# Kernel optimization log

Measured on AMD Instinct MI355X. Metric: run time of the kernel, lower is better.

Reference implementation:

```python
import jax, jax.numpy as jnp
from jax import lax
import numpy as np

NUM_CLASSES = 80
STRIDES = (8, 16, 32)
CONF_THRE = 0.01
NMS_THRE = 0.65
TOPK = 500  # fixed pre-NMS candidate cap (jit-compatible stand-in for dynamic conf filter)


def setup_inputs() -> dict:
    key = jax.random.key(0)
    k8, k16, k32 = jax.random.split(key, 3)
    B, C = 8, 5 + NUM_CLASSES
    return {
        "out8": jax.random.normal(k8, (B, C, 160, 160), dtype=jnp.float32),
        "out16": jax.random.normal(k16, (B, C, 80, 80), dtype=jnp.float32),
        "out32": jax.random.normal(k32, (B, C, 40, 40), dtype=jnp.float32),
    }


def _decode_level(x, stride):
    # x: [B, C, H, W] -> decoded [B, H*W, C]
    B, C, H, W = x.shape
    x = x.reshape(B, C, H * W).transpose(0, 2, 1)  # [B, HW, C]
    yv, xv = jnp.meshgrid(jnp.arange(H), jnp.arange(W), indexing="ij")
    grid = jnp.stack([xv, yv], axis=-1).reshape(1, H * W, 2).astype(x.dtype)
    s = jnp.asarray(stride, x.dtype)
    xy = (x[..., 0:2] + grid) * s
    wh = jnp.exp(x[..., 2:4]) * s
    obj = jax.nn.sigmoid(x[..., 4:5])
    cls = jax.nn.sigmoid(x[..., 5:])
    return jnp.concatenate([xy, wh, obj, cls], axis=-1)


def _iou_one_vs_all(box, boxes):
    # box: [4] xyxy, boxes: [K,4] xyxy
    x1 = jnp.maximum(box[0], boxes[:, 0])
    y1 = jnp.maximum(box[1], boxes[:, 1])
    x2 = jnp.minimum(box[2], boxes[:, 2])
    y2 = jnp.minimum(box[3], boxes[:, 3])
    inter = jnp.maximum(x2 - x1, 0.0) * jnp.maximum(y2 - y1, 0.0)
    a1 = jnp.maximum(box[2] - box[0], 0.0) * jnp.maximum(box[3] - box[1], 0.0)
    a2 = jnp.maximum(boxes[:, 2] - boxes[:, 0], 0.0) * jnp.maximum(boxes[:, 3] - boxes[:, 1], 0.0)
    return inter / (a1 + a2 - inter + 1e-9)


def _nms_keep(boxes, valid, iou_thr):
    # boxes are pre-sorted by descending score; returns bool keep mask [K]
    K = boxes.shape[0]
    idx = jnp.arange(K)

    def body(i, state):
        keep, suppressed = state
        cur_ok = jnp.logical_not(suppressed[i])
        keep = keep.at[i].set(cur_ok)
        iou = _iou_one_vs_all(boxes[i], boxes)
        suppressed = suppressed | ((iou > iou_thr) & cur_ok & (idx > i))
        return keep, suppressed

    keep, _ = lax.fori_loop(0, K, body, (jnp.zeros(K, bool), jnp.logical_not(valid)))
    return keep


def _post_process_image(pred):
    # pred: [N, 5+num_classes] decoded, boxes already xyxy
    cls_scores = pred[:, 5:5 + NUM_CLASSES]
    class_conf = jnp.max(cls_scores, axis=1)
    class_pred = jnp.argmax(cls_scores, axis=1)
    obj = pred[:, 4]
    total = obj * class_conf  # NMS score, same as torchvision call
    masked = jnp.where(total >= CONF_THRE, total, -1.0)
    top_sc, top_i = lax.top_k(masked, TOPK)  # sorted descending
    boxes = pred[top_i, :4]
    obj_k = obj[top_i]
    cc_k = class_conf[top_i]
    lab_k = class_pred[top_i]
    valid = top_sc >= CONF_THRE
    # class-aware (batched) NMS via per-class coordinate offset, as torchvision does
    max_c = jnp.max(jnp.where(valid[:, None], boxes, 0.0)) + 1.0
    boxes_off = boxes + (lab_k.astype(boxes.dtype) * max_c)[:, None]
    keep = _nms_keep(boxes_off, valid, NMS_THRE)
    det = jnp.concatenate(
        [boxes, obj_k[:, None], cc_k[:, None], lab_k.astype(boxes.dtype)[:, None]], axis=1
    )  # [K, 7] = (x1,y1,x2,y2,obj,class_conf,class_id)
    return det * keep[:, None].astype(det.dtype)


def reference(out8, out16, out32):
    levels = [(out8, 8), (out16, 16), (out32, 32)]
    pred = jnp.concatenate([_decode_level(x, s) for x, s in levels], axis=1)  # [B, N, C]
    # cxcywh -> xyxy corners
    cx, cy, w, h = pred[..., 0], pred[..., 1], pred[..., 2], pred[..., 3]
    corners = jnp.stack([cx - w / 2, cy - h / 2, cx + w / 2, cy + h / 2], axis=-1)
    pred = jnp.concatenate([corners, pred[..., 4:]], axis=-1)
    return jax.vmap(_post_process_image)(pred)  # [B, TOPK, 7], zero-padded
```

## Files before the change

### kernel.cpp

```cpp
#include <hip/hip_runtime.h>

#define NPI    33600
#define KTOP   500
#define CAP    1024
#define KEY001 0xBC23D70Au
#define NGRP   1024
#define NIMG   8
#define GPW    525

__device__ __forceinline__ float sigmoidf_(float x) {
  return 1.0f / (1.0f + expf(-x));
}
__device__ __forceinline__ unsigned fkey(float f) {
  unsigned u = __float_as_uint(f);
  return (u & 0x80000000u) ? ~u : (u | 0x80000000u);
}

__global__ __launch_bounds__(256) void k_score(
    const float* __restrict__ p8, const float* __restrict__ p16,
    const float* __restrict__ p32,
    unsigned* __restrict__ keys, unsigned* __restrict__ hist2)
{
  const int b  = blockIdx.y;
  const int tx = blockIdx.x;
  const float* lvl; int HW, j0, abase;
  if (tx < 50)      { lvl = p8;  HW = 25600; j0 = tx * 512;        abase = 0; }
  else if (tx < 63) { lvl = p16; HW = 6400;  j0 = (tx - 50) * 512; abase = 25600; }
  else              { lvl = p32; HW = 1600;  j0 = (tx - 63) * 512; abase = 32000; }
  __shared__ unsigned lh[NGRP];
  for (int i = threadIdx.x; i < NGRP; i += 256) lh[i] = 0;
  __syncthreads();

  const int e = j0 + 2 * threadIdx.x;
  if (e < HW) {
    const float* base = lvl + (size_t)b * 85 * HW + e;
    float2 o2 = *(const float2*)(base + (size_t)4 * HW);
    float m0 = -INFINITY, m1 = -INFINITY;
    for (int c0 = 5; c0 < 85; c0 += 16) {
      float2 r[16];
      #pragma unroll
      for (int u = 0; u < 16; ++u)
        r[u] = *(const float2*)(base + (size_t)(c0 + u) * HW);
      #pragma unroll
      for (int u = 0; u < 16; ++u) { m0 = fmaxf(m0, r[u].x); m1 = fmaxf(m1, r[u].y); }
    }
    float s0 = sigmoidf_(o2.x) * sigmoidf_(m0);
    float s1 = sigmoidf_(o2.y) * sigmoidf_(m1);
    unsigned k0 = fkey(s0 >= 0.01f ? s0 : -1.0f);
    unsigned k1 = fkey(s1 >= 0.01f ? s1 : -1.0f);
    *(uint2*)(keys + (size_t)b * NPI + abase + e) = make_uint2(k0, k1);
    atomicAdd(&lh[k0 >> 22], 1u);
    atomicAdd(&lh[k1 >> 22], 1u);
  }
  __syncthreads();
  unsigned* gb = hist2 + (size_t)b * NGRP;
  for (int i = threadIdx.x; i < NGRP; i += 256) {
    unsigned v = lh[i];
    if (v) atomicAdd(&gb[i], v);
  }
}

__global__ __launch_bounds__(1024) void k_select(
    const unsigned* __restrict__ hist2, const unsigned* __restrict__ keys,
    unsigned* __restrict__ selanch, unsigned* __restrict__ invalg)
{
  const int b    = blockIdx.x;
  const int tid  = threadIdx.x;
  const int lane = tid & 63;
  const int wave = tid >> 6;

  __shared__ unsigned lh[NGRP];
  __shared__ unsigned sh_sub[4096];
  __shared__ unsigned sh_c64[64];
  __shared__ unsigned sh_G, sh_T;
  __shared__ __align__(16) unsigned long long sh_cand[CAP];
  __shared__ unsigned sh_inval[16];
  __shared__ unsigned sh_wcA[16], sh_wcB[16];

  lh[tid] = hist2[(size_t)b * NGRP + tid];
  for (int i = tid; i < 4096; i += 1024) sh_sub[i] = 0;
  __syncthreads();
  if (tid < 64) {
    unsigned s = 0;
    #pragma unroll
    for (int k = 0; k < 16; ++k) s += lh[tid * 16 + k];
    sh_c64[tid] = s;
  }
  __syncthreads();
  if (tid == 0) {
    unsigned cum = 0; int C = 0;
    for (int g = 63; g >= 0; --g) {
      unsigned v = sh_c64[g];
      if (cum + v >= KTOP) { C = g; break; }
      cum += v;
    }
    int G = C * 16; unsigned chi = cum;
    for (int g = C * 16 + 15; g >= C * 16; --g) {
      unsigned v = lh[g];
      if (chi + v >= KTOP) { G = g; break; }
      chi += v;
    }
    sh_G = (unsigned)G;
    sh_c64[0] = chi;
  }
  __syncthreads();
  const unsigned G = sh_G;
  const unsigned* kb = keys + (size_t)b * NPI;

  for (int g = tid; g < NPI / 4; g += 1024) {
    uint4 kv = ((const uint4*)kb)[g];
    unsigned kk[4] = {kv.x, kv.y, kv.z, kv.w};
    #pragma unroll
    for (int q = 0; q < 4; ++q)
      if ((kk[q] >> 22) == G) atomicAdd(&sh_sub[(kk[q] >> 10) & 4095u], 1u);
  }
  __syncthreads();
  unsigned chi10 = sh_c64[0];
  __syncthreads();
  if (tid < 64) {
    unsigned s = 0;
    for (int k = 0; k < 64; ++k) s += sh_sub[tid * 64 + k];
    sh_c64[tid] = s;
  }
  __syncthreads();
  if (tid == 0) {
    unsigned c = chi10; int C2 = 0;
    for (int g = 63; g >= 0; --g) {
      unsigned v = sh_c64[g];
      if (c + v >= KTOP) { C2 = g; break; }
      c += v;
    }
    int T12 = C2 * 64;
    for (int t2 = C2 * 64 + 63; t2 >= C2 * 64; --t2) {
      unsigned v = sh_sub[t2];
      if (c + v >= KTOP) { T12 = t2; break; }
      c += v;
    }
    sh_T = (G << 12) | (unsigned)T12;
  }
  __syncthreads();
  const unsigned T = sh_T;

  unsigned runA = 0, runB = 0;
  for (int it = 0; it < 9; ++it) {
    int gl = it * 64 + lane;
    bool act = (gl < GPW);
    int g = wave * GPW + gl;
    uint4 kv = act ? ((const uint4*)kb)[g] : make_uint4(0, 0, 0, 0);
    unsigned kk[4] = {kv.x, kv.y, kv.z, kv.w};
    #pragma unroll
    for (int q = 0; q < 4; ++q) {
      unsigned bin = kk[q] >> 10;
      runA += (unsigned)__popcll(__ballot(act && (bin > T)));
      runB += (unsigned)__popcll(__ballot(act && (bin == T)));
    }
  }
  if (lane == 0) { sh_wcA[wave] = runA; sh_wcB[wave] = runB; }
  __syncthreads();
  unsigned pA = 0, pB = 0, nA = 0, nBtot = 0;
  #pragma unroll
  for (int w2 = 0; w2 < 16; ++w2) {
    unsigned va = sh_wcA[w2], vb = sh_wcB[w2];
    if (w2 < wave) { pA += va; pB += vb; }
    nA += va; nBtot += vb;
  }
  const unsigned Bcap = CAP - nA;
  const unsigned nBk  = (nBtot < Bcap) ? nBtot : Bcap;
  const int nTot = (int)(nA + nBk);

  for (int it = 0; it < 9; ++it) {
    int gl = it * 64 + lane;
    bool act = (gl < GPW);
    int g = wave * GPW + gl;
    uint4 kv = act ? ((const uint4*)kb)[g] : make_uint4(0, 0, 0, 0);
    unsigned kk[4] = {kv.x, kv.y, kv.z, kv.w};
    bool iA[4], iB[4];
    unsigned long long balA[4], balB[4];
    #pragma unroll
    for (int q = 0; q < 4; ++q) {
      unsigned bin = kk[q] >> 10;
      iA[q] = act && (bin > T);
      iB[q] = act && (bin == T);
      balA[q] = __ballot(iA[q]);
      balB[q] = __ballot(iB[q]);
    }
    unsigned long long lt = (1ULL << lane) - 1ULL;
    unsigned pAl = pA, pBl = pB;
    #pragma unroll
    for (int q = 0; q < 4; ++q) {
      pAl += (unsigned)__popcll(balA[q] & lt);
      pBl += (unsigned)__popcll(balB[q] & lt);
    }
    #pragma unroll
    for (int q = 0; q < 4; ++q) {
      int a0 = g * 4 + q;
      unsigned long long packed =
          ((unsigned long long)kk[q] << 32) |
          (unsigned long long)(0xFFFFFFFFu - (unsigned)a0);
      if (iA[q]) { sh_cand[pAl] = packed; ++pAl; }
      if (iB[q]) { if (pBl < Bcap) sh_cand[nA + pBl] = packed; ++pBl; }
      pA += (unsigned)__popcll(balA[q]);
      pB += (unsigned)__popcll(balB[q]);
    }
  }
  __syncthreads();
  for (int s = nTot + tid; s < CAP; s += 1024) sh_cand[s] = 0ULL;
  __syncthreads();

  for (unsigned kk2 = 2; kk2 <= CAP; kk2 <<= 1) {
    for (unsigned jj = kk2 >> 1; jj > 0; jj >>= 1) {
      unsigned i = (unsigned)tid, p = i ^ jj;
      if (p > i) {
        unsigned long long x = sh_cand[i], y = sh_cand[p];
        bool desc = ((i & kk2) == 0);
        if ((x < y) == desc) { sh_cand[i] = y; sh_cand[p] = x; }
      }
      __syncthreads();
    }
  }

  if (tid < KTOP) {
    unsigned long long v = sh_cand[tid];
    unsigned keyk = (unsigned)(v >> 32);
    int a = (int)(0xFFFFFFFFu - (unsigned)(v & 0xFFFFFFFFull));
    if (a < 0) a = 0;
    selanch[b * KTOP + tid] = (unsigned)a;
    bool validk = (keyk >= KEY001);
    unsigned long long bv = __ballot(!validk);
    if (lane == 0) {
      sh_inval[wave * 2]     = (unsigned)(bv & 0xFFFFFFFFull);
      sh_inval[wave * 2 + 1] = (unsigned)(bv >> 32);
    }
  } else {
    unsigned long long bv = __ballot(false);
    (void)bv;
  }
  __syncthreads();
  if (tid < 16) invalg[b * 16 + tid] = sh_inval[tid];
}

__global__ __launch_bounds__(256) void k_gather(
    const float* __restrict__ p8, const float* __restrict__ p16,
    const float* __restrict__ p32,
    const unsigned* __restrict__ selanch, float* __restrict__ seldet)
{
  const int b    = blockIdx.y;
  const int part = blockIdx.x;
  const int tid  = threadIdx.x;
  const int p    = tid & 15;
  const int grp  = tid >> 4;
  const int lane = tid & 63;
  const int g0   = lane & ~15;

  for (int iter = 0; iter < 4; ++iter) {
    int s = part * 64 + iter * 16 + grp;
    if (s >= KTOP) continue;
    int a = (int)selanch[b * KTOP + s];
    const float* lvl; int j, W, HW, S;
    if (a < 25600)      { lvl = p8;  j = a;         W = 160; HW = 25600; S = 8;  }
    else if (a < 32000) { lvl = p16; j = a - 25600; W = 80;  HW = 6400;  S = 16; }
    else                { lvl = p32; j = a - 32000; W = 40;  HW = 1600;  S = 32; }
    const float* base = lvl + (size_t)b * 85 * HW + j;
    float cc = -1.0f; int lab = 0;
    #pragma unroll
    for (int u = 0; u < 5; ++u) {
      int c = p + 16 * u;
      float sv = sigmoidf_(base[(size_t)(5 + c) * HW]);
      if (sv > cc) { cc = sv; lab = c; }
    }
    float tload = (p < 5) ? base[(size_t)p * HW] : 0.0f;
    #pragma unroll
    for (int off = 1; off < 16; off <<= 1) {
      float occ = __shfl_xor(cc, off);
      int  olb = __shfl_xor(lab, off);
      if (occ > cc || (occ == cc && olb < lab)) { cc = occ; lab = olb; }
    }
    float t0 = __shfl(tload, g0 + 0);
    float t1 = __shfl(tload, g0 + 1);
    float t2 = __shfl(tload, g0 + 2);
    float t3 = __shfl(tload, g0 + 3);
    float t4 = __shfl(tload, g0 + 4);
    if (p == 0) {
      int gy = j / W, gx = j - gy * W;
      float fs = (float)S;
      float cx = (t0 + (float)gx) * fs;
      float cy = (t1 + (float)gy) * fs;
      float w  = expf(t2) * fs;
      float h  = expf(t3) * fs;
      float obj = sigmoidf_(t4);
      float* d = seldet + ((size_t)b * KTOP + s) * 7;
      d[0] = cx - 0.5f * w; d[1] = cy - 0.5f * h;
      d[2] = cx + 0.5f * w; d[3] = cy + 0.5f * h;
      d[4] = obj; d[5] = cc; d[6] = (float)lab;
    }
  }
}

__global__ __launch_bounds__(256) void k_iou(
    const float* __restrict__ seldet, const unsigned* __restrict__ invalg,
    unsigned* __restrict__ gmask)
{
  const int w = blockIdx.x, b = blockIdx.y;
  const int tid = threadIdx.x;
  const int lane = tid & 63;
  const int wave = tid >> 6;
  __shared__ float sd[KTOP * 7];
  __shared__ float sx1[512], sy1[512], sx2[512], sy2[512], sa[512];
  __shared__ float sred[4];
  __shared__ float smaxc;
  for (int x = tid; x < KTOP * 7; x += 256)
    sd[x] = seldet[(size_t)b * (KTOP * 7) + x];
  __syncthreads();
  float contrib = 0.0f;
  for (int i = tid; i < KTOP; i += 256) {
    bool valid = ((invalg[b * 16 + (i >> 5)] >> (i & 31)) & 1u) == 0u;
    float m4 = fmaxf(fmaxf(sd[i * 7 + 0], sd[i * 7 + 1]),
                     fmaxf(sd[i * 7 + 2], sd[i * 7 + 3]));
    contrib = fmaxf(contrib, valid ? m4 : 0.0f);
  }
  #pragma unroll
  for (int off = 32; off > 0; off >>= 1) contrib = fmaxf(contrib, __shfl_xor(contrib, off));
  if (lane == 0) sred[wave] = contrib;
  __syncthreads();
  if (tid == 0) smaxc = fmaxf(fmaxf(sred[0], sred[1]), fmaxf(sred[2], sred[3])) + 1.0f;
  __syncthreads();
  const float maxc = smaxc;
  for (int i = tid; i < 512; i += 256) {
    float x1, y1, x2, y2, ar;
    if (i < KTOP) {
      float offb = sd[i * 7 + 6] * maxc;
      x1 = sd[i * 7 + 0] + offb; y1 = sd[i * 7 + 1] + offb;
      x2 = sd[i * 7 + 2] + offb; y2 = sd[i * 7 + 3] + offb;
      ar = fmaxf(x2 - x1, 0.0f) * fmaxf(y2 - y1, 0.0f);
    } else { x1 = y1 = x2 = y2 = ar = 0.0f; }
    sx1[i] = x1; sy1[i] = y1; sx2[i] = x2; sy2[i] = y2; sa[i] = ar;
  }
  __syncthreads();
  const int jbase = w * 32;
  for (int i = tid; i < KTOP; i += 256) {
    unsigned bits = 0u;
    if (jbase + 31 > i) {
      float ix1 = sx1[i], iy1 = sy1[i], ix2 = sx2[i], iy2 = sy2[i];
      float a1 = sa[i];
      #pragma unroll 4
      for (int jj = 0; jj < 32; ++jj) {
        int j = jbase + jj;
        if (j < KTOP && j > i) {
          float jx1 = sx1[j], jy1 = sy1[j];
          float jx2 = sx2[j], jy2 = sy2[j];
          float a2  = sa[j];
          float iw = fminf(ix2, jx2) - fmaxf(ix1, jx1);
          float ih = fminf(iy2, jy2) - fmaxf(iy1, jy1);
          float inter = fmaxf(iw, 0.0f) * fmaxf(ih, 0.0f);
          if (inter > 0.65f * (a1 + a2 - inter + 1e-9f)) bits |= (1u << jj);
        }
      }
    }
    gmask[((size_t)b * 16 + w) * 512 + i] = bits;
  }
}

__global__ __launch_bounds__(256) void k_nms(
    const unsigned* __restrict__ gmask, const unsigned* __restrict__ invalg,
    const float* __restrict__ seldet, float* __restrict__ out)
{
  const int b = blockIdx.x;
  const int tid = threadIdx.x;
  const int lane = tid & 63;
  __shared__ unsigned sm[KTOP * 17];
  __shared__ unsigned sh_keep[16];
  for (int g = tid; g < KTOP * 16; g += 256) {
    int w = g / KTOP, i = g - w * KTOP;
    sm[i * 17 + w] = gmask[((size_t)b * 16 + w) * 512 + i];
  }
  __syncthreads();
  if (tid < 64) {
    unsigned sup   = (lane < 16) ? invalg[b * 16 + lane] : 0u;
    unsigned keepw = 0u;
    unsigned cur = (unsigned)__builtin_amdgcn_readlane((int)sup, 0);
    unsigned mA = (lane < 16) ? sm[0 * 17 + lane] : 0u;
    unsigned mB = (lane < 16) ? sm[1 * 17 + lane] : 0u;
    for (int i = 0; i < KTOP; i += 2) {
      bool ok = ((cur >> (i & 31)) & 1u) == 0u;
      if (ok) {
        sup |= mA;
        if (lane == (i >> 5)) keepw |= (1u << (i & 31));
      }
      cur = (unsigned)__builtin_amdgcn_readlane((int)sup, (i + 1) >> 5);
      mA = (lane < 16 && (i + 2) < KTOP) ? sm[(i + 2) * 17 + lane] : 0u;
      bool ok2 = ((cur >> ((i + 1) & 31)) & 1u) == 0u;
      if (ok2) {
        sup |= mB;
        if (lane == ((i + 1) >> 5)) keepw |= (1u << ((i + 1) & 31));
      }
      cur = (unsigned)__builtin_amdgcn_readlane((int)sup, (i + 2) >> 5);
      mB = (lane < 16 && (i + 3) < KTOP) ? sm[(i + 3) * 17 + lane] : 0u;
    }
    if (lane < 16) sh_keep[lane] = keepw;
  }
  __syncthreads();
  for (int x = tid; x < KTOP * 7; x += 256) {
    int k = x / 7;
    float keepf = ((sh_keep[k >> 5] >> (k & 31)) & 1u) ? 1.0f : 0.0f;
    out[(size_t)b * (KTOP * 7) + x] = seldet[(size_t)b * (KTOP * 7) + x] * keepf;
  }
}

extern "C" void kernel_launch(void* const* d_in, const int* in_sizes, int n_in,
                              void* d_out, int out_size, void* d_ws, size_t ws_size,
                              hipStream_t stream) {
  const float* p8  = (const float*)d_in[0];
  const float* p16 = (const float*)d_in[1];
  const float* p32 = (const float*)d_in[2];
  float* out = (float*)d_out;
  unsigned* hist2   = (unsigned*)d_ws;
  unsigned* keys    = hist2 + (size_t)NIMG * NGRP;
  unsigned* selanch = keys + (size_t)NIMG * NPI;
  unsigned* invalg  = selanch + (size_t)NIMG * KTOP;
  unsigned* gmask   = invalg + NIMG * 16;
  float*    seldet  = (float*)(gmask + (size_t)NIMG * 16 * 512);

  hipMemsetAsync(hist2, 0, (size_t)NIMG * NGRP * 4, stream);
  k_score <<<dim3(67, NIMG), 256, 0, stream>>>(p8, p16, p32, keys, hist2);
  k_select<<<dim3(NIMG), 1024, 0, stream>>>(hist2, keys, selanch, invalg);
  k_gather<<<dim3(8, NIMG), 256, 0, stream>>>(p8, p16, p32, selanch, seldet);
  k_iou   <<<dim3(16, NIMG), 256, 0, stream>>>(seldet, invalg, gmask);
  k_nms   <<<dim3(NIMG), 256, 0, stream>>>(gmask, invalg, seldet, out);
}
```

Measured before the change: 201.9 us.

## Replace global histogram atomics with per-block partials and streamline top-K selection

k_score now handles four anchors per thread with float4 loads across half as many blocks. Each block writes its own partial histogram row, which removes the memset and the global atomics. k_select runs with 512 threads and sums the partial rows itself. It finds thresholds with wave-level shuffle scans instead of single-thread serial loops, and compacts candidates in one pass using shared atomic counters. The boundary bin goes to a side buffer, with a fallback slow path when that overflows, and the bitonic sort can shrink to 512 when there are few candidates. The cost is extra partial-histogram traffic, and candidate order within a bin is no longer deterministic before sorting, but the sort key includes the anchor index.

```diff
diff --git a/kernel.cpp b/kernel.cpp
--- a/kernel.cpp
+++ b/kernel.cpp
@@ -6,7 +6,8 @@
 #define KEY001 0xBC23D70Au
 #define NGRP   1024
 #define NIMG   8
-#define GPW    525
+#define NBLK   34
+#define BCAPB  528
 
 __device__ __forceinline__ float sigmoidf_(float x) {
   return 1.0f / (1.0f + expf(-x));
@@ -19,49 +20,53 @@
 __global__ __launch_bounds__(256) void k_score(
     const float* __restrict__ p8, const float* __restrict__ p16,
     const float* __restrict__ p32,
-    unsigned* __restrict__ keys, unsigned* __restrict__ hist2)
+    unsigned* __restrict__ keys, unsigned* __restrict__ histp)
 {
   const int b  = blockIdx.y;
-  const int tx = blockIdx.x;
+  const int xb = blockIdx.x;
   const float* lvl; int HW, j0, abase;
-  if (tx < 50)      { lvl = p8;  HW = 25600; j0 = tx * 512;        abase = 0; }
-  else if (tx < 63) { lvl = p16; HW = 6400;  j0 = (tx - 50) * 512; abase = 25600; }
-  else              { lvl = p32; HW = 1600;  j0 = (tx - 63) * 512; abase = 32000; }
+  if (xb < 25)      { lvl = p8;  HW = 25600; j0 = xb * 1024;        abase = 0; }
+  else if (xb < 32) { lvl = p16; HW = 6400;  j0 = (xb - 25) * 1024; abase = 25600; }
+  else              { lvl = p32; HW = 1600;  j0 = (xb - 32) * 1024; abase = 32000; }
   __shared__ unsigned lh[NGRP];
   for (int i = threadIdx.x; i < NGRP; i += 256) lh[i] = 0;
   __syncthreads();
 
-  const int e = j0 + 2 * threadIdx.x;
+  const int e = j0 + 4 * threadIdx.x;
   if (e < HW) {
     const float* base = lvl + (size_t)b * 85 * HW + e;
-    float2 o2 = *(const float2*)(base + (size_t)4 * HW);
-    float m0 = -INFINITY, m1 = -INFINITY;
+    float4 o4 = *(const float4*)(base + (size_t)4 * HW);
+    float m0 = -INFINITY, m1 = -INFINITY, m2 = -INFINITY, m3 = -INFINITY;
     for (int c0 = 5; c0 < 85; c0 += 16) {
-      float2 r[16];
+      float4 r[16];
       #pragma unroll
       for (int u = 0; u < 16; ++u)
-        r[u] = *(const float2*)(base + (size_t)(c0 + u) * HW);
+        r[u] = *(const float4*)(base + (size_t)(c0 + u) * HW);
       #pragma unroll
-      for (int u = 0; u < 16; ++u) { m0 = fmaxf(m0, r[u].x); m1 = fmaxf(m1, r[u].y); }
-    }
-    float s0 = sigmoidf_(o2.x) * sigmoidf_(m0);
-    float s1 = sigmoidf_(o2.y) * sigmoidf_(m1);
-    unsigned k0 = fkey(s0 >= 0.01f ? s0 : -1.0f);
-    unsigned k1 = fkey(s1 >= 0.01f ? s1 : -1.0f);
-    *(uint2*)(keys + (size_t)b * NPI + abase + e) = make_uint2(k0, k1);
-    atomicAdd(&lh[k0 >> 22], 1u);
-    atomicAdd(&lh[k1 >> 22], 1u);
-  }
-  __syncthreads();
-  unsigned* gb = hist2 + (size_t)b * NGRP;
-  for (int i = threadIdx.x; i < NGRP; i += 256) {
-    unsigned v = lh[i];
-    if (v) atomicAdd(&gb[i], v);
-  }
-}
-
-__global__ __launch_bounds__(1024) void k_select(
-    const unsigned* __restrict__ hist2, const unsigned* __restrict__ keys,
+      for (int u = 0; u < 16; ++u) {
+        m0 = fmaxf(m0, r[u].x); m1 = fmaxf(m1, r[u].y);
+        m2 = fmaxf(m2, r[u].z); m3 = fmaxf(m3, r[u].w);
+      }
+    }
+    float ov[4] = {o4.x, o4.y, o4.z, o4.w};
+    float mv[4] = {m0, m1, m2, m3};
+    unsigned k4[4];
+    #pragma unroll
+    for (int q = 0; q < 4; ++q) {
+      float s = sigmoidf_(ov[q]) * sigmoidf_(mv[q]);
+      k4[q] = fkey(s >= 0.01f ? s : -1.0f);
+    }
+    *(uint4*)(keys + (size_t)b * NPI + abase + e) = make_uint4(k4[0], k4[1], k4[2], k4[3]);
+    #pragma unroll
+    for (int q = 0; q < 4; ++q) atomicAdd(&lh[k4[q] >> 22], 1u);
+  }
+  __syncthreads();
+  unsigned* gb = histp + ((size_t)b * NBLK + xb) * NGRP;
+  for (int i = threadIdx.x; i < NGRP; i += 256) gb[i] = lh[i];
+}
+
+__global__ __launch_bounds__(512) void k_select(
+    const unsigned* __restrict__ histp, const unsigned* __restrict__ keys,
     unsigned* __restrict__ selanch, unsigned* __restrict__ invalg)
 {
   const int b    = blockIdx.x;
@@ -72,42 +77,62 @@
   __shared__ unsigned lh[NGRP];
   __shared__ unsigned sh_sub[4096];
   __shared__ unsigned sh_c64[64];
-  __shared__ unsigned sh_G, sh_T;
+  __shared__ unsigned sh_G, sh_chi10, sh_T;
+  __shared__ int sh_ctrA, sh_ctrB;
   __shared__ __align__(16) unsigned long long sh_cand[CAP];
+  __shared__ __align__(16) unsigned long long sh_candB[BCAPB];
   __shared__ unsigned sh_inval[16];
-  __shared__ unsigned sh_wcA[16], sh_wcB[16];
-
-  lh[tid] = hist2[(size_t)b * NGRP + tid];
-  for (int i = tid; i < 4096; i += 1024) sh_sub[i] = 0;
+  __shared__ unsigned sh_wcB[8];
+
+  {
+    unsigned s0 = 0, s1 = 0;
+    for (int r = 0; r < NBLK; ++r) {
+      const unsigned* row = histp + ((size_t)b * NBLK + r) * NGRP;
+      s0 += row[tid]; s1 += row[tid + 512];
+    }
+    lh[tid] = s0; lh[tid + 512] = s1;
+  }
+  for (int i = tid; i < 4096; i += 512) sh_sub[i] = 0;
+  if (tid == 0) { sh_ctrA = 0; sh_ctrB = 0; }
   __syncthreads();
   if (tid < 64) {
     unsigned s = 0;
     #pragma unroll
-    for (int k = 0; k < 16; ++k) s += lh[tid * 16 + k];
+    for (int k = 0; k < 16; ++k) s += lh[tid * 16 + ((k + tid) & 15)];
     sh_c64[tid] = s;
   }
   __syncthreads();
-  if (tid == 0) {
-    unsigned cum = 0; int C = 0;
-    for (int g = 63; g >= 0; --g) {
-      unsigned v = sh_c64[g];
-      if (cum + v >= KTOP) { C = g; break; }
-      cum += v;
-    }
-    int G = C * 16; unsigned chi = cum;
-    for (int g = C * 16 + 15; g >= C * 16; --g) {
-      unsigned v = lh[g];
-      if (chi + v >= KTOP) { G = g; break; }
-      chi += v;
-    }
-    sh_G = (unsigned)G;
-    sh_c64[0] = chi;
+  if (wave == 0) {
+    unsigned v = sh_c64[lane];
+    unsigned t = v;
+    #pragma unroll
+    for (int off = 1; off < 64; off <<= 1) {
+      unsigned o = (unsigned)__shfl_down((int)t, off);
+      if (lane + off < 64) t += o;
+    }
+    unsigned long long m = __ballot(t >= KTOP);
+    int C = 63 - __builtin_clzll(m);
+    unsigned cumAfter = (unsigned)__shfl((int)t, C) - (unsigned)__shfl((int)v, C);
+    unsigned v2 = (lane < 16) ? lh[C * 16 + lane] : 0u;
+    unsigned t2 = v2;
+    #pragma unroll
+    for (int off = 1; off < 16; off <<= 1) {
+      unsigned o = (unsigned)__shfl_down((int)t2, off);
+      if (lane + off < 16) t2 += o;
+    }
+    t2 += cumAfter;
+    unsigned long long m2 = __ballot((lane < 16) && (t2 >= KTOP));
+    int Gl = 63 - __builtin_clzll(m2);
+    if (lane == 0) {
+      sh_G = (unsigned)(C * 16 + Gl);
+      sh_chi10 = (unsigned)__shfl((int)t2, Gl) - (unsigned)__shfl((int)v2, Gl);
+    }
   }
   __syncthreads();
   const unsigned G = sh_G;
   const unsigned* kb = keys + (size_t)b * NPI;
 
-  for (int g = tid; g < NPI / 4; g += 1024) {
+  for (int g = tid; g < NPI / 4; g += 512) {
     uint4 kv = ((const uint4*)kb)[g];
     unsigned kk[4] = {kv.x, kv.y, kv.z, kv.w};
     #pragma unroll
@@ -115,67 +140,48 @@
       if ((kk[q] >> 22) == G) atomicAdd(&sh_sub[(kk[q] >> 10) & 4095u], 1u);
   }
   __syncthreads();
-  unsigned chi10 = sh_c64[0];
-  __syncthreads();
   if (tid < 64) {
     unsigned s = 0;
-    for (int k = 0; k < 64; ++k) s += sh_sub[tid * 64 + k];
+    for (int k = 0; k < 64; ++k) s += sh_sub[tid * 64 + ((k + tid) & 63)];
     sh_c64[tid] = s;
   }
   __syncthreads();
-  if (tid == 0) {
-    unsigned c = chi10; int C2 = 0;
-    for (int g = 63; g >= 0; --g) {
-      unsigned v = sh_c64[g];
-      if (c + v >= KTOP) { C2 = g; break; }
-      c += v;
-    }
-    int T12 = C2 * 64;
-    for (int t2 = C2 * 64 + 63; t2 >= C2 * 64; --t2) {
-      unsigned v = sh_sub[t2];
-      if (c + v >= KTOP) { T12 = t2; break; }
-      c += v;
-    }
-    sh_T = (G << 12) | (unsigned)T12;
+  if (wave == 0) {
+    unsigned chi10 = sh_chi10;
+    unsigned v = sh_c64[lane];
+    unsigned t = v;
+    #pragma unroll
+    for (int off = 1; off < 64; off <<= 1) {
+      unsigned o = (unsigned)__shfl_down((int)t, off);
+      if (lane + off < 64) t += o;
+    }
+    t += chi10;
+    unsigned long long m = __ballot(t >= KTOP);
+    int C2 = 63 - __builtin_clzll(m);
+    unsigned after = (unsigned)__shfl((int)t, C2) - (unsigned)__shfl((int)v, C2);
+    unsigned v3 = sh_sub[C2 * 64 + lane];
+    unsigned t3 = v3;
+    #pragma unroll
+    for (int off = 1; off < 64; off <<= 1) {
+      unsigned o = (unsigned)__shfl_down((int)t3, off);
+      if (lane + off < 64) t3 += o;
+    }
+    t3 += after;
+    unsigned long long m3 = __ballot(t3 >= KTOP);
+    int Gl = 63 - __builtin_clzll(m3);
+    if (lane == 0) sh_T = (G << 12) | (unsigned)(C2 * 64 + Gl);
   }
   __syncthreads();
   const unsigned T = sh_T;
 
-  unsigned runA = 0, runB = 0;
-  for (int it = 0; it < 9; ++it) {
-    int gl = it * 64 + lane;
-    bool act = (gl < GPW);
-    int g = wave * GPW + gl;
-    uint4 kv = act ? ((const uint4*)kb)[g] : make_uint4(0, 0, 0, 0);
-    unsigned kk[4] = {kv.x, kv.y, kv.z, kv.w};
-    #pragma unroll
-    for (int q = 0; q < 4; ++q) {
-      unsigned bin = kk[q] >> 10;
-      runA += (unsigned)__popcll(__ballot(act && (bin > T)));
-      runB += (unsigned)__popcll(__ballot(act && (bin == T)));
-    }
-  }
-  if (lane == 0) { sh_wcA[wave] = runA; sh_wcB[wave] = runB; }
-  __syncthreads();
-  unsigned pA = 0, pB = 0, nA = 0, nBtot = 0;
-  #pragma unroll
-  for (int w2 = 0; w2 < 16; ++w2) {
-    unsigned va = sh_wcA[w2], vb = sh_wcB[w2];
-    if (w2 < wave) { pA += va; pB += vb; }
-    nA += va; nBtot += vb;
-  }
-  const unsigned Bcap = CAP - nA;
-  const unsigned nBk  = (nBtot < Bcap) ? nBtot : Bcap;
-  const int nTot = (int)(nA + nBk);
-
-  for (int it = 0; it < 9; ++it) {
-    int gl = it * 64 + lane;
-    bool act = (gl < GPW);
-    int g = wave * GPW + gl;
+  for (int it = 0; it < 17; ++it) {
+    int g = it * 512 + tid;
+    bool act = (g < NPI / 4);
     uint4 kv = act ? ((const uint4*)kb)[g] : make_uint4(0, 0, 0, 0);
     unsigned kk[4] = {kv.x, kv.y, kv.z, kv.w};
     bool iA[4], iB[4];
     unsigned long long balA[4], balB[4];
+    unsigned tA = 0, tB = 0;
     #pragma unroll
     for (int q = 0; q < 4; ++q) {
       unsigned bin = kk[q] >> 10;
@@ -183,57 +189,113 @@
       iB[q] = act && (bin == T);
       balA[q] = __ballot(iA[q]);
       balB[q] = __ballot(iB[q]);
-    }
+      tA += (unsigned)__popcll(balA[q]);
+      tB += (unsigned)__popcll(balB[q]);
+    }
+    int bA = 0, bB = 0;
+    if (lane == 0) {
+      if (tA) bA = atomicAdd(&sh_ctrA, (int)tA);
+      if (tB) bB = atomicAdd(&sh_ctrB, (int)tB);
+    }
+    bA = __shfl(bA, 0); bB = __shfl(bB, 0);
     unsigned long long lt = (1ULL << lane) - 1ULL;
-    unsigned pAl = pA, pBl = pB;
+    unsigned offA = 0, offB = 0;
     #pragma unroll
     for (int q = 0; q < 4; ++q) {
-      pAl += (unsigned)__popcll(balA[q] & lt);
-      pBl += (unsigned)__popcll(balB[q] & lt);
-    }
-    #pragma unroll
-    for (int q = 0; q < 4; ++q) {
-      int a0 = g * 4 + q;
+      unsigned posA = (unsigned)bA + offA + (unsigned)__popcll(balA[q] & lt);
+      unsigned posB = (unsigned)bB + offB + (unsigned)__popcll(balB[q] & lt);
       unsigned long long packed =
           ((unsigned long long)kk[q] << 32) |
-          (unsigned long long)(0xFFFFFFFFu - (unsigned)a0);
-      if (iA[q]) { sh_cand[pAl] = packed; ++pAl; }
-      if (iB[q]) { if (pBl < Bcap) sh_cand[nA + pBl] = packed; ++pBl; }
-      pA += (unsigned)__popcll(balA[q]);
-      pB += (unsigned)__popcll(balB[q]);
-    }
-  }
-  __syncthreads();
-  for (int s = nTot + tid; s < CAP; s += 1024) sh_cand[s] = 0ULL;
-  __syncthreads();
-
-  for (unsigned kk2 = 2; kk2 <= CAP; kk2 <<= 1) {
-    for (unsigned jj = kk2 >> 1; jj > 0; jj >>= 1) {
-      unsigned i = (unsigned)tid, p = i ^ jj;
-      if (p > i) {
-        unsigned long long x = sh_cand[i], y = sh_cand[p];
-        bool desc = ((i & kk2) == 0);
-        if ((x < y) == desc) { sh_cand[i] = y; sh_cand[p] = x; }
-      }
-      __syncthreads();
-    }
-  }
-
+          (unsigned long long)(0xFFFFFFFFu - (unsigned)(g * 4 + q));
+      if (iA[q]) sh_cand[posA] = packed;
+      if (iB[q] && posB < BCAPB) sh_candB[posB] = packed;
+      offA += (unsigned)__popcll(balA[q]);
+      offB += (unsigned)__popcll(balB[q]);
+    }
+  }
+  __syncthreads();
+  const int nA    = sh_ctrA;
+  const int nBtot = sh_ctrB;
+  const int Bcap  = CAP - nA;
+  const bool fast = (nBtot <= Bcap) && (nBtot <= BCAPB);
+  int nBk;
+  if (fast) {
+    nBk = nBtot;
+    for (int i2 = tid; i2 < nBtot; i2 += 512) sh_cand[nA + i2] = sh_candB[i2];
+  } else {
+    nBk = (nBtot < Bcap) ? nBtot : Bcap;
+    const int GPW2 = NPI / 4 / 8;
+    unsigned runB = 0;
+    for (int it = 0; it < 17; ++it) {
+      int gl = it * 64 + lane;
+      bool act = (gl < GPW2);
+      int g = wave * GPW2 + gl;
+      uint4 kv = act ? ((const uint4*)kb)[g] : make_uint4(0, 0, 0, 0);
+      unsigned kk[4] = {kv.x, kv.y, kv.z, kv.w};
+      #pragma unroll
+      for (int q = 0; q < 4; ++q)
+        runB += (unsigned)__popcll(__ballot(act && ((kk[q] >> 10) == T)));
+    }
+    if (lane == 0) sh_wcB[wave] = runB;
+    __syncthreads();
+    unsigned pB = 0;
+    for (int w2 = 0; w2 < wave; ++w2) pB += sh_wcB[w2];
+    for (int it = 0; it < 17; ++it) {
+      int gl = it * 64 + lane;
+      bool act = (gl < GPW2);
+      int g = wave * GPW2 + gl;
+      uint4 kv = act ? ((const uint4*)kb)[g] : make_uint4(0, 0, 0, 0);
+      unsigned kk[4] = {kv.x, kv.y, kv.z, kv.w};
+      unsigned long long lt = (1ULL << lane) - 1ULL;
+      #pragma unroll
+      for (int q = 0; q < 4; ++q) {
+        bool iB = act && ((kk[q] >> 10) == T);
+        unsigned long long bal = __ballot(iB);
+        unsigned pBl = pB + (unsigned)__popcll(bal & lt);
+        if (iB && pBl < (unsigned)Bcap) {
+          sh_cand[nA + pBl] =
+              ((unsigned long long)kk[q] << 32) |
+              (unsigned long long)(0xFFFFFFFFu - (unsigned)(g * 4 + q));
+        }
+        pB += (unsigned)__popcll(bal);
+      }
+    }
+  }
+  const int nTot = nA + nBk;
+  const int P = (nTot <= 512) ? 512 : 1024;
+  __syncthreads();
+  for (int s = nTot + tid; s < P; s += 512) sh_cand[s] = 0ULL;
+  __syncthreads();
+
+  {
+    const int half = P >> 1;
+    for (unsigned kk2 = 2; kk2 <= (unsigned)P; kk2 <<= 1) {
+      for (unsigned jj = kk2 >> 1; jj > 0; jj >>= 1) {
+        if (tid < half) {
+          unsigned i = (((unsigned)tid & ~(jj - 1)) << 1) | ((unsigned)tid & (jj - 1));
+          unsigned p = i | jj;
+          unsigned long long x = sh_cand[i], y = sh_cand[p];
+          bool desc = ((i & kk2) == 0);
+          if ((x < y) == desc) { sh_cand[i] = y; sh_cand[p] = x; }
+        }
+        __syncthreads();
+      }
+    }
+  }
+
+  bool validk = false;
   if (tid < KTOP) {
     unsigned long long v = sh_cand[tid];
     unsigned keyk = (unsigned)(v >> 32);
     int a = (int)(0xFFFFFFFFu - (unsigned)(v & 0xFFFFFFFFull));
     if (a < 0) a = 0;
     selanch[b * KTOP + tid] = (unsigned)a;
-    bool validk = (keyk >= KEY001);
-    unsigned long long bv = __ballot(!validk);
-    if (lane == 0) {
-      sh_inval[wave * 2]     = (unsigned)(bv & 0xFFFFFFFFull);
-      sh_inval[wave * 2 + 1] = (unsigned)(bv >> 32);
-    }
-  } else {
-    unsigned long long bv = __ballot(false);
-    (void)bv;
+    validk = (keyk >= KEY001);
+  }
+  unsigned long long bv = __ballot((tid < KTOP) && !validk);
+  if (lane == 0) {
+    sh_inval[wave * 2]     = (unsigned)(bv & 0xFFFFFFFFull);
+    sh_inval[wave * 2 + 1] = (unsigned)(bv >> 32);
   }
   __syncthreads();
   if (tid < 16) invalg[b * 16 + tid] = sh_inval[tid];
@@ -413,16 +475,15 @@
   const float* p16 = (const float*)d_in[1];
   const float* p32 = (const float*)d_in[2];
   float* out = (float*)d_out;
-  unsigned* hist2   = (unsigned*)d_ws;
-  unsigned* keys    = hist2 + (size_t)NIMG * NGRP;
+  unsigned* histp   = (unsigned*)d_ws;
+  unsigned* keys    = histp + (size_t)NIMG * NBLK * NGRP;
   unsigned* selanch = keys + (size_t)NIMG * NPI;
   unsigned* invalg  = selanch + (size_t)NIMG * KTOP;
   unsigned* gmask   = invalg + NIMG * 16;
   float*    seldet  = (float*)(gmask + (size_t)NIMG * 16 * 512);
 
-  hipMemsetAsync(hist2, 0, (size_t)NIMG * NGRP * 4, stream);
-  k_score <<<dim3(67, NIMG), 256, 0, stream>>>(p8, p16, p32, keys, hist2);
-  k_select<<<dim3(NIMG), 1024, 0, stream>>>(hist2, keys, selanch, invalg);
+  k_score <<<dim3(NBLK, NIMG), 256, 0, stream>>>(p8, p16, p32, keys, histp);
+  k_select<<<dim3(NIMG), 512, 0, stream>>>(histp, keys, selanch, invalg);
   k_gather<<<dim3(8, NIMG), 256, 0, stream>>>(p8, p16, p32, selanch, seldet);
   k_iou   <<<dim3(16, NIMG), 256, 0, stream>>>(seldet, invalg, gmask);
   k_nms   <<<dim3(NIMG), 256, 0, stream>>>(gmask, invalg, seldet, out);
```

Result: no change. 205.5 us (+1.8%).
